# Kernel tuning notes

Hardware: AMD Instinct MI355X
Metric: run time of the kernel (lower is better)

Reference implementation:

```python
import jax, jax.numpy as jnp
import numpy as np

P = 1.0  # Yager t-norm exponent (tnorm_p)


def _patches(x, k):
    # x: [B, C, H, W] -> [B, C*k*k, Ho, Wo], feature ordering (c, kh, kw) like torch unfold
    B, C, H, W = x.shape
    Ho, Wo = H - k + 1, W - k + 1
    cols = [x[:, :, i:i + Ho, j:j + Wo] for i in range(k) for j in range(k)]
    p = jnp.stack(cols, axis=2)  # [B, C, k*k, Ho, Wo]
    return p.reshape(B, C * k * k, Ho, Wo)


def _max_yager2d(x, w, p):
    # Fuzzy conv: Yager t-norm T(a,b)=max(0, 1-((1-a)^p+(1-b)^p)^(1/p)) between each
    # patch element and kernel weight, aggregated with max over the receptive field.
    O, C, k, _ = w.shape
    pat = _patches(x, k)                       # [B, L, Ho, Wo], L = C*k*k
    wf = w.reshape(O, -1)                      # [O, L]
    a = 1.0 - pat[:, None]                     # [B, 1, L, Ho, Wo]
    b = 1.0 - wf[None, :, :, None, None]       # [1, O, L, 1, 1]
    t = jnp.maximum(0.0, 1.0 - (a ** p + b ** p) ** (1.0 / p))
    return jnp.max(t, axis=2)                  # [B, O, Ho, Wo]


def _maxpool2(x):
    return jax.lax.reduce_window(x, -jnp.inf, jax.lax.max,
                                 (1, 1, 2, 2), (1, 1, 2, 2), 'VALID')


def setup_inputs() -> dict:
    key = jax.random.key(0)
    k1, k2, k3, k4, k5, k6, k7 = jax.random.split(key, 7)
    B = 128
    inputs = jax.random.uniform(k1, (B, 3, 32, 32), dtype=jnp.float32)
    # fuzzy kernels are membership values in [0,1]
    w1 = jax.random.uniform(k2, (6, 3, 5, 5), dtype=jnp.float32)
    w2 = jax.random.uniform(k3, (16, 6, 5, 5), dtype=jnp.float32)
    w3 = jax.random.uniform(k4, (120, 16, 5, 5), dtype=jnp.float32)
    wd = jax.random.normal(k5, (120, 84), dtype=jnp.float32) * 0.1  # DenseDefuzzy weights
    wf = jax.random.normal(k6, (84, 10), dtype=jnp.float32) * 0.1   # fc5 weight
    bf = jax.random.normal(k7, (10,), dtype=jnp.float32) * 0.01     # fc5 bias
    return {"inputs": inputs, "w1": w1, "w2": w2, "w3": w3,
            "wd": wd, "wf": wf, "bf": bf}


def reference(inputs, w1, w2, w3, wd, wf, bf):
    x = _maxpool2(_max_yager2d(inputs, w1, P))   # [B,6,14,14]
    x = _maxpool2(_max_yager2d(x, w2, P))        # [B,16,5,5]
    x = _max_yager2d(x, w3, P)                   # [B,120,1,1]
    x = x.reshape(x.shape[0], -1)                # [B,120]
    x = jnp.tanh(x @ wd)                         # DenseDefuzzy (unnormalized) + tanh
    return jax.nn.log_softmax(x @ wf + bf, axis=-1)
```

## Files before the change

### kernel.cpp

```cpp
#include <hip/hip_runtime.h>
#include <math.h>


#define NT 1024
#define ROWS 34
#define PLANE (32 * ROWS)

__global__ __launch_bounds__(NT) void fused_lenet(
    const float* __restrict__ x,
    const float* __restrict__ w1,
    const float* __restrict__ w2,
    const float* __restrict__ w3,
    const float* __restrict__ wd,
    const float* __restrict__ wf,
    const float* __restrict__ bfv,
    float* __restrict__ out)
{
    const int img = blockIdx.x;
    const int tid = threadIdx.x;

    __shared__ float s_in[3 * PLANE];
    __shared__ float s_w1d[648];
    __shared__ float s_w2d[3456];
    __shared__ float s_w2r[2400];
    __shared__ float s_wf[850];
    __shared__ unsigned s_a1u[1176];
    __shared__ unsigned s_a2u[400];
    __shared__ float s_a3[120];
    __shared__ float s_a4[84];

    float4 w3p[13];
    if (tid < 960) {
        const int o = tid >> 3, q = tid & 7;
        const float4* wv = (const float4*)(w3 + o * 400);
        #pragma unroll
        for (int i = 0; i < 13; ++i) {
            int l = q + 8 * i; if (l > 99) l = 99;
            w3p[i] = wv[l];
        }
    }

    {
        const float2* src = (const float2*)(x + img * 3072);
        for (int i = tid; i < 1536; i += NT) {
            const int c = i >> 9, rem = i & 511, r = rem >> 4, col2 = rem & 15;
            ((float2*)s_in)[c * (PLANE / 2) + r * (ROWS / 2) + col2] = src[i];
        }
        for (int i = tid; i < 1200; i += NT)
            ((float2*)s_w2r)[i] = ((const float2*)w2)[i];
        if (tid < 850)
            s_wf[tid] = (tid < 840) ? wf[tid] : bfv[tid - 840];
        for (int i = tid; i < 1176; i += NT) s_a1u[i] = 0u;
        if (tid < 400) s_a2u[tid] = 0u;
        if (tid < 648) {
            const int oc = tid / 108, u = tid - oc * 108;
            const int c = u / 36, v = u - c * 36;
            const int r = v / 6, col = v - r * 6;
            const float* raw = w1 + (oc * 3 + c) * 25;
            float m = -1e30f;
            #pragma unroll
            for (int dy = 0; dy < 2; ++dy) {
                const int kh = r - dy;
                if ((unsigned)kh > 4u) continue;
                #pragma unroll
                for (int dx = 0; dx < 2; ++dx) {
                    const int kw = col - dx;
                    if ((unsigned)kw > 4u) continue;
                    m = fmaxf(m, raw[kh * 5 + kw]);
                }
            }
            s_w1d[tid] = m;
        }
    }
    __syncthreads();

    if (tid < 1008) {
        const int c = tid / 336;
        const int rr = tid - c * 336;
        const int oc = rr / 56;
        const int r2 = rr - oc * 56;
        const int py = r2 >> 2;
        const int s = (r2 >> 1) & 1;
        const int h = r2 & 1;
        float acc[7];
        #pragma unroll
        for (int j = 0; j < 7; ++j) acc[j] = -1e30f;
        const float* wbase = s_w1d + (oc * 3 + c) * 36 + h * 18;
        const float* xbase = s_in + c * PLANE + (2 * py + 3 * h) * ROWS + 14 * s;
        #pragma unroll
        for (int u = 0; u < 3; ++u) {
            const float* xr = xbase + u * ROWS;
            float xv[18];
            #pragma unroll
            for (int i2 = 0; i2 < 9; ++i2)
                ((float2*)xv)[i2] = ((const float2*)xr)[i2];
            float wv[6];
            #pragma unroll
            for (int i2 = 0; i2 < 3; ++i2)
                ((float2*)wv)[i2] = ((const float2*)(wbase + u * 6))[i2];
            #pragma unroll
            for (int j = 0; j < 7; ++j) {
                #pragma unroll
                for (int ux = 0; ux < 6; ++ux)
                    acc[j] = fmaxf(acc[j], xv[2 * j + ux] + wv[ux]);
            }
        }
        const int obase = oc * 196 + py * 14 + 7 * s;
        #pragma unroll
        for (int j = 0; j < 7; ++j) {
            const float rl = fmaxf(acc[j] - 1.0f, 0.0f);
            atomicMax(&s_a1u[obase + j], __float_as_uint(rl));
        }
    }
    for (int e = tid; e < 3456; e += NT) {
        const int oc = e / 216, u = e - oc * 216;
        const int c = u / 36, v = u - c * 36;
        const int r = v / 6, col = v - r * 6;
        const float* raw = s_w2r + (oc * 6 + c) * 25;
        float m = -1e30f;
        #pragma unroll
        for (int dy = 0; dy < 2; ++dy) {
            const int kh = r - dy;
            if ((unsigned)kh > 4u) continue;
            #pragma unroll
            for (int dx = 0; dx < 2; ++dx) {
                const int kw = col - dx;
                if ((unsigned)kw > 4u) continue;
                m = fmaxf(m, raw[kh * 5 + kw]);
            }
        }
        s_w2d[e] = m;
    }
    __syncthreads();

    if (tid < 960) {
        const int oc = tid / 60;
        const int rr = tid - oc * 60;
        const int py = rr / 12;
        const int r2 = rr - py * 12;
        const int c = r2 >> 1;
        const int h = r2 & 1;
        float acc[5];
        #pragma unroll
        for (int j = 0; j < 5; ++j) acc[j] = -1e30f;
        const float* a1f = (const float*)s_a1u;
        const float* wbase = s_w2d + (oc * 6 + c) * 36 + h * 18;
        const float* xbase = a1f + c * 196 + (2 * py + 3 * h) * 14;
        #pragma unroll
        for (int u = 0; u < 3; ++u) {
            const float* xr = xbase + u * 14;
            float xv[14];
            #pragma unroll
            for (int i2 = 0; i2 < 7; ++i2)
                ((float2*)xv)[i2] = ((const float2*)xr)[i2];
            float wv[6];
            #pragma unroll
            for (int i2 = 0; i2 < 3; ++i2)
                ((float2*)wv)[i2] = ((const float2*)(wbase + u * 6))[i2];
            #pragma unroll
            for (int j = 0; j < 5; ++j) {
                #pragma unroll
                for (int ux = 0; ux < 6; ++ux)
                    acc[j] = fmaxf(acc[j], xv[2 * j + ux] + wv[ux]);
            }
        }
        const int obase = oc * 25 + py * 5;
        #pragma unroll
        for (int j = 0; j < 5; ++j) {
            const float rl = fmaxf(acc[j] - 1.0f, 0.0f);
            atomicMax(&s_a2u[obase + j], __float_as_uint(rl));
        }
    }
    float wdp[15];
    if (tid < 672) {
        const int o = tid >> 3, q = tid & 7;
        #pragma unroll
        for (int i = 0; i < 15; ++i)
            wdp[i] = wd[(q * 15 + i) * 84 + o];
    }
    __syncthreads();

    if (tid < 960) {
        const int o = tid >> 3, q = tid & 7;
        const float4* av = (const float4*)(const float*)s_a2u;
        float m = -1e30f;
        #pragma unroll
        for (int i = 0; i < 13; ++i) {
            int l = q + 8 * i; if (l > 99) l = 99;
            const float4 a = av[l];
            const float4 w = w3p[i];
            m = fmaxf(m, fmaxf(fmaxf(a.x + w.x, a.y + w.y),
                               fmaxf(a.z + w.z, a.w + w.w)));
        }
        m = fmaxf(m, __shfl_xor(m, 1));
        m = fmaxf(m, __shfl_xor(m, 2));
        m = fmaxf(m, __shfl_xor(m, 4));
        if (q == 0) s_a3[o] = fmaxf(m - 1.0f, 0.0f);
    }
    __syncthreads();

    if (tid < 672) {
        const int o = tid >> 3, q = tid & 7;
        float acc = 0.0f;
        #pragma unroll
        for (int i = 0; i < 15; ++i)
            acc = fmaf(s_a3[q * 15 + i], wdp[i], acc);
        acc += __shfl_xor(acc, 1);
        acc += __shfl_xor(acc, 2);
        acc += __shfl_xor(acc, 4);
        if (q == 0) s_a4[o] = tanhf(acc);
    }
    __syncthreads();

    if (tid < 64) {
        float acc = 0.0f;
        if (tid < 40) {
            const int o = tid >> 2, q = tid & 3;
            #pragma unroll 7
            for (int i = 0; i < 21; ++i) {
                const int k = q * 21 + i;
                acc = fmaf(s_a4[k], s_wf[k * 10 + o], acc);
            }
            acc += __shfl_xor(acc, 1);
            acc += __shfl_xor(acc, 2);
            acc += s_wf[840 + o];
        }
        const float lg = __shfl(acc, (tid < 10) ? tid * 4 : 0);
        if (tid < 16) {
            float v = (tid < 10) ? lg : -1e30f;
            #pragma unroll
            for (int d = 1; d < 16; d <<= 1)
                v = fmaxf(v, __shfl_xor(v, d));
            float e = (tid < 10) ? expf(lg - v) : 0.0f;
            float ssum = e;
            #pragma unroll
            for (int d = 1; d < 16; d <<= 1)
                ssum += __shfl_xor(ssum, d);
            if (tid < 10)
                out[img * 10 + tid] = lg - v - logf(ssum);
        }
    }
}

extern "C" void kernel_launch(void* const* d_in, const int* in_sizes, int n_in,
                              void* d_out, int out_size, void* d_ws, size_t ws_size,
                              hipStream_t stream) {
    const float* x   = (const float*)d_in[0];
    const float* w1  = (const float*)d_in[1];
    const float* w2  = (const float*)d_in[2];
    const float* w3  = (const float*)d_in[3];
    const float* wd  = (const float*)d_in[4];
    const float* wf  = (const float*)d_in[5];
    const float* bfv = (const float*)d_in[6];
    float* out = (float*)d_out;

    const int B = in_sizes[0] / (3 * 32 * 32);
    fused_lenet<<<dim3(B), dim3(NT), 0, stream>>>(
        x, w1, w2, w3, wd, wf, bfv, out);
}
```

Before: 77.16 us.

## Register-block conv1/conv2 over output channels and defer w3 prefetch

Each conv1 thread now computes 3 output channels and each conv2 thread 4, so the loaded input row is reused across channels from registers. This cuts LDS input reads per output, and conv1 and conv2 now use 336 and 240 active threads instead of about 1000. The w3 register prefetch moves after conv1 so fewer registers are live during conv1. The cost is less parallelism per block and more serial work per thread, with larger per-thread accumulator arrays.

```diff
diff --git a/kernel.cpp b/kernel.cpp
--- a/kernel.cpp
+++ b/kernel.cpp
@@ -30,15 +30,6 @@
     __shared__ float s_a4[84];
 
     float4 w3p[13];
-    if (tid < 960) {
-        const int o = tid >> 3, q = tid & 7;
-        const float4* wv = (const float4*)(w3 + o * 400);
-        #pragma unroll
-        for (int i = 0; i < 13; ++i) {
-            int l = q + 8 * i; if (l > 99) l = 99;
-            w3p[i] = wv[l];
-        }
-    }
 
     {
         const float2* src = (const float2*)(x + img * 3072);
@@ -74,42 +65,59 @@
     }
     __syncthreads();
 
-    if (tid < 1008) {
-        const int c = tid / 336;
-        const int rr = tid - c * 336;
-        const int oc = rr / 56;
-        const int r2 = rr - oc * 56;
+    if (tid < 336) {
+        const int c = tid / 112;
+        const int r = tid - c * 112;
+        const int ocg = r / 56;
+        const int r2 = r - ocg * 56;
         const int py = r2 >> 2;
         const int s = (r2 >> 1) & 1;
         const int h = r2 & 1;
-        float acc[7];
-        #pragma unroll
-        for (int j = 0; j < 7; ++j) acc[j] = -1e30f;
-        const float* wbase = s_w1d + (oc * 3 + c) * 36 + h * 18;
+        float acc[3][7];
+        #pragma unroll
+        for (int o = 0; o < 3; ++o)
+            #pragma unroll
+            for (int j = 0; j < 7; ++j) acc[o][j] = -1e30f;
         const float* xbase = s_in + c * PLANE + (2 * py + 3 * h) * ROWS + 14 * s;
         #pragma unroll
         for (int u = 0; u < 3; ++u) {
-            const float* xr = xbase + u * ROWS;
             float xv[18];
             #pragma unroll
             for (int i2 = 0; i2 < 9; ++i2)
-                ((float2*)xv)[i2] = ((const float2*)xr)[i2];
-            float wv[6];
-            #pragma unroll
-            for (int i2 = 0; i2 < 3; ++i2)
-                ((float2*)wv)[i2] = ((const float2*)(wbase + u * 6))[i2];
+                ((float2*)xv)[i2] = ((const float2*)(xbase + u * ROWS))[i2];
+            #pragma unroll
+            for (int o = 0; o < 3; ++o) {
+                const float* wbase =
+                    s_w1d + ((ocg * 3 + o) * 3 + c) * 36 + h * 18 + u * 6;
+                float wv[6];
+                #pragma unroll
+                for (int i2 = 0; i2 < 3; ++i2)
+                    ((float2*)wv)[i2] = ((const float2*)wbase)[i2];
+                #pragma unroll
+                for (int j = 0; j < 7; ++j) {
+                    #pragma unroll
+                    for (int ux = 0; ux < 6; ++ux)
+                        acc[o][j] = fmaxf(acc[o][j], xv[2 * j + ux] + wv[ux]);
+                }
+            }
+        }
+        #pragma unroll
+        for (int o = 0; o < 3; ++o) {
+            const int obase = (ocg * 3 + o) * 196 + py * 14 + 7 * s;
             #pragma unroll
             for (int j = 0; j < 7; ++j) {
-                #pragma unroll
-                for (int ux = 0; ux < 6; ++ux)
-                    acc[j] = fmaxf(acc[j], xv[2 * j + ux] + wv[ux]);
-            }
-        }
-        const int obase = oc * 196 + py * 14 + 7 * s;
-        #pragma unroll
-        for (int j = 0; j < 7; ++j) {
-            const float rl = fmaxf(acc[j] - 1.0f, 0.0f);
-            atomicMax(&s_a1u[obase + j], __float_as_uint(rl));
+                const float rl = fmaxf(acc[o][j] - 1.0f, 0.0f);
+                atomicMax(&s_a1u[obase + j], __float_as_uint(rl));
+            }
+        }
+    }
+    if (tid < 960) {
+        const int o = tid >> 3, q = tid & 7;
+        const float4* wv = (const float4*)(w3 + o * 400);
+        #pragma unroll
+        for (int i = 0; i < 13; ++i) {
+            int l = q + 8 * i; if (l > 99) l = 99;
+            w3p[i] = wv[l];
         }
     }
     for (int e = tid; e < 3456; e += NT) {
@@ -133,42 +141,50 @@
     }
     __syncthreads();
 
-    if (tid < 960) {
-        const int oc = tid / 60;
-        const int rr = tid - oc * 60;
-        const int py = rr / 12;
-        const int r2 = rr - py * 12;
+    if (tid < 240) {
+        const int ocq = tid / 60;
+        const int r = tid - ocq * 60;
+        const int py = r / 12;
+        const int r2 = r - py * 12;
         const int c = r2 >> 1;
         const int h = r2 & 1;
-        float acc[5];
-        #pragma unroll
-        for (int j = 0; j < 5; ++j) acc[j] = -1e30f;
+        float acc[4][5];
+        #pragma unroll
+        for (int o = 0; o < 4; ++o)
+            #pragma unroll
+            for (int j = 0; j < 5; ++j) acc[o][j] = -1e30f;
         const float* a1f = (const float*)s_a1u;
-        const float* wbase = s_w2d + (oc * 6 + c) * 36 + h * 18;
         const float* xbase = a1f + c * 196 + (2 * py + 3 * h) * 14;
         #pragma unroll
         for (int u = 0; u < 3; ++u) {
-            const float* xr = xbase + u * 14;
             float xv[14];
             #pragma unroll
             for (int i2 = 0; i2 < 7; ++i2)
-                ((float2*)xv)[i2] = ((const float2*)xr)[i2];
-            float wv[6];
-            #pragma unroll
-            for (int i2 = 0; i2 < 3; ++i2)
-                ((float2*)wv)[i2] = ((const float2*)(wbase + u * 6))[i2];
+                ((float2*)xv)[i2] = ((const float2*)(xbase + u * 14))[i2];
+            #pragma unroll
+            for (int o = 0; o < 4; ++o) {
+                const float* wbase =
+                    s_w2d + ((ocq * 4 + o) * 6 + c) * 36 + h * 18 + u * 6;
+                float wv[6];
+                #pragma unroll
+                for (int i2 = 0; i2 < 3; ++i2)
+                    ((float2*)wv)[i2] = ((const float2*)wbase)[i2];
+                #pragma unroll
+                for (int j = 0; j < 5; ++j) {
+                    #pragma unroll
+                    for (int ux = 0; ux < 6; ++ux)
+                        acc[o][j] = fmaxf(acc[o][j], xv[2 * j + ux] + wv[ux]);
+                }
+            }
+        }
+        #pragma unroll
+        for (int o = 0; o < 4; ++o) {
+            const int obase = (ocq * 4 + o) * 25 + py * 5;
             #pragma unroll
             for (int j = 0; j < 5; ++j) {
-                #pragma unroll
-                for (int ux = 0; ux < 6; ++ux)
-                    acc[j] = fmaxf(acc[j], xv[2 * j + ux] + wv[ux]);
-            }
-        }
-        const int obase = oc * 25 + py * 5;
-        #pragma unroll
-        for (int j = 0; j < 5; ++j) {
-            const float rl = fmaxf(acc[j] - 1.0f, 0.0f);
-            atomicMax(&s_a2u[obase + j], __float_as_uint(rl));
+                const float rl = fmaxf(acc[o][j] - 1.0f, 0.0f);
+                atomicMax(&s_a2u[obase + j], __float_as_uint(rl));
+            }
         }
     }
     float wdp[15];
```

Result: no change. 75.80 us (-1.8%).
